# Performance work log

Hardware: AMD Instinct MI355X
Metric: run time of the kernel (lower is better)

The kernel has to match this reference:

```python
import jax, jax.numpy as jnp
import numpy as np

TEMP = 20.0
NEG = -1.0e9


def l2norm(x, eps=1e-12):
    # F.normalize(p=2, dim=-1): x / max(||x||, eps)
    n = jnp.sqrt(jnp.sum(x * x, axis=-1, keepdims=True))
    return x / jnp.maximum(n, eps)


def setup_inputs() -> dict:
    key = jax.random.key(0)
    ks = jax.random.split(key, 8)
    Bv, Lv, Dv = 32, 196, 768
    Bt, Lt, Dt = 32, 64, 768
    D = 512
    inp = {
        "visual_feature": jax.random.normal(ks[0], (Bv, Lv, Dv), jnp.float32),
        "textual_feature": jax.random.normal(ks[1], (Bt, Lt, Dt), jnp.float32),
        "mask": jax.random.randint(ks[2], (Bt, Lt), 0, 2, jnp.int32),
        "W_vis": jax.random.normal(ks[3], (D, Dv), jnp.float32) * (2.0 / D) ** 0.5,
        "b_vis": jnp.zeros((D,), jnp.float32),
        "W_txt": jax.random.normal(ks[4], (D, Dt), jnp.float32) * (2.0 / D) ** 0.5,
        "b_txt": jnp.zeros((D,), jnp.float32),
        "W_qs": jax.random.normal(ks[5], (D, D), jnp.float32) * (2.0 / D) ** 0.5,
        "W_ks": jax.random.normal(ks[6], (D, D), jnp.float32) * (2.0 / D) ** 0.5,
    }
    return inp


def _mha(q_in, k_in, v_in, k_mask, W_qs, W_ks):
    # all-pairs cross attention (n_head == 1), vectorized over the original
    # per-sample Python loop: output [Bk, Bq, Lq, Dv]
    q = l2norm(jnp.einsum('qld,ed->qle', q_in, W_qs))  # [Bq, Lq, D]
    k = l2norm(jnp.einsum('kmd,ed->kme', k_in, W_ks))  # [Bk, Lk, D]
    attn = jnp.einsum('qle,kme->kqlm', q, k)           # [Bk, Bq, Lq, Lk]
    attn = jax.nn.relu(attn) * TEMP
    if k_mask is not None:
        attn = jnp.where(k_mask[:, None, None, :] == 1, NEG, attn)
    attn = jax.nn.softmax(attn, axis=-1)
    return jnp.einsum('kqlm,kmd->kqld', attn, v_in)    # [Bk, Bq, Lq, Dv]


def reference(visual_feature, textual_feature, mask, W_vis, b_vis, W_txt, b_txt, W_qs, W_ks):
    visual_embed = jnp.einsum('bld,ed->ble', visual_feature, W_vis) + b_vis   # [Bv,Lv,D]
    textual_embed = jnp.einsum('bld,ed->ble', textual_feature, W_txt) + b_txt # [Bt,Lt,D]
    visual_norm = l2norm(visual_embed)
    textual_norm = l2norm(textual_embed)
    # q=visual, k/v=textual, masked by text padding -> [Bt, Bv, Lv, D]
    att_text = _mha(visual_norm, textual_norm, textual_embed, mask, W_qs, W_ks)
    # q=textual, k/v=visual, no mask -> [Bv, Bt, Lt, D]
    att_vis = _mha(textual_norm, visual_norm, visual_embed, None, W_qs, W_ks)
    att_text = l2norm(att_text)
    att_vis = l2norm(att_vis)
    # att_vis_feat[:, mask == 1, :] = 0
    att_vis = att_vis * (mask == 0)[None, :, :, None].astype(att_vis.dtype)
    # matmul(att_text [t,v,l,d], att_vis.permute(1,0,3,2) [t,v,d,m]) -> mean(2,3)
    sim = jnp.einsum('tvld,vtmd->tvlm', att_text, att_vis)
    return sim.mean(axis=(2, 3))  # [Bt, Bv]
```

## Files before the change

### kernel.cpp

```cpp
#include <hip/hip_runtime.h>
#include <math.h>

#define BV 32
#define LV 196
#define DV 768
#define BT 32
#define LT 64
#define DD 512
#define MV (BV*LV)
#define MT (BT*LT)
#define TEMPF 20.0f
#define NEGF  -1.0e9f

typedef unsigned short u16;
typedef unsigned int   u32;
typedef short bf16x8 __attribute__((ext_vector_type(8)));
typedef float f32x4  __attribute__((ext_vector_type(4)));

__device__ __forceinline__ u16 f2bf(float f) {
    u32 u = __float_as_uint(f);
    u32 r = u + 0x7fffu + ((u >> 16) & 1u);
    return (u16)(r >> 16);
}
__device__ __forceinline__ float bf2f(u16 h) { return __uint_as_float(((u32)h) << 16); }

__device__ __forceinline__ size_t tiled_chunk_off(int m, int kk, int KB2) {
    int rowBlk = m >> 7, row = m & 127;
    int kBlk = kk >> 6, ke = kk & 63;
    return ((size_t)(rowBlk * KB2 + kBlk) << 13) + row * 64 + ((((ke >> 3) ^ (row & 7)) << 4) >> 1);
}

__global__ __launch_bounds__(256)
void conv_split(const float* __restrict__ X, u16* __restrict__ X2, int M, int K)
{
    int gid = blockIdx.x * 256 + threadIdx.x;
    int perRow = K >> 3;
    if (gid >= M * perRow) return;
    int m = gid / perRow, k8 = (gid - m * perRow) << 3;
    const float* xp = X + (size_t)m * K + k8;
    float x[8];
    *(float4*)&x[0] = *(const float4*)xp;
    *(float4*)&x[4] = *(const float4*)(xp + 4);
    union { u16 h[8]; uint4 v; } hi, lo;
    #pragma unroll
    for (int e = 0; e < 8; ++e) {
        hi.h[e] = f2bf(x[e]);
        lo.h[e] = f2bf(x[e] - bf2f(hi.h[e]));
    }
    int KB2 = K >> 5;
    *(uint4*)&X2[tiled_chunk_off(m, k8, KB2)]     = hi.v;
    *(uint4*)&X2[tiled_chunk_off(m, K + k8, KB2)] = lo.v;
}

__global__ __launch_bounds__(256)
void rownorm_conv(const float* __restrict__ X, u16* __restrict__ X2, int M)
{
    const int row  = blockIdx.x * 4 + (threadIdx.x >> 6);
    const int lane = threadIdx.x & 63;
    const float* ip = X + (size_t)row * DD + lane * 8;
    float x[8];
    *(float4*)&x[0] = *(const float4*)ip;
    *(float4*)&x[4] = *(const float4*)(ip + 4);
    float ss = 0.f;
    #pragma unroll
    for (int e = 0; e < 8; ++e) ss += x[e] * x[e];
    #pragma unroll
    for (int off = 32; off; off >>= 1) ss += __shfl_xor(ss, off, 64);
    const float inv = 1.f / fmaxf(sqrtf(ss), 1e-12f);
    union { u16 h[8]; uint4 v; } hi, lo;
    #pragma unroll
    for (int e = 0; e < 8; ++e) {
        float xv = x[e] * inv;
        hi.h[e] = f2bf(xv);
        lo.h[e] = f2bf(xv - bf2f(hi.h[e]));
    }
    const int k8 = lane * 8, KB2 = 16;
    *(uint4*)&X2[tiled_chunk_off(row, k8, KB2)]       = hi.v;
    *(uint4*)&X2[tiled_chunk_off(row, DD + k8, KB2)]  = lo.v;
}

__device__ __forceinline__ void gload16(const u16* g, u16* l) {
    __builtin_amdgcn_global_load_lds((const __attribute__((address_space(1))) u32*)g,
                                     (__attribute__((address_space(3))) u32*)l, 16, 0, 0);
}

__global__ __launch_bounds__(256, 2)
void gemm_split_nt(const u16* __restrict__ A2, const u16* __restrict__ B2,
                   const float* __restrict__ bias, float* __restrict__ C,
                   int M, int N, int K, int hasBias)
{
    const int KB  = K >> 6;
    const int KB2 = KB * 2;
    const int bm = blockIdx.y, bn = blockIdx.x;
    const int tid = threadIdx.x;
    const int w = tid >> 6, lane = tid & 63;
    const int wr = (w >> 1) << 6, wc = (w & 1) << 6;
    const int fr = lane & 15, fq = lane >> 4;

    __shared__ u16 As[2][8192];
    __shared__ u16 Bs[2][8192];

    f32x4 acc[4][4];
    #pragma unroll
    for (int i = 0; i < 4; ++i)
        #pragma unroll
        for (int j = 0; j < 4; ++j) acc[i][j] = (f32x4){0.f, 0.f, 0.f, 0.f};

    const int swz = (fr & 7) << 4;
    const int aoff0 = ((wr + fr) << 7) >> 1;
    const int boff0 = ((wc + fr) << 7) >> 1;
    const int k0 = ((fq << 4) ^ swz) >> 1;
    const int k1 = ((64 + (fq << 4)) ^ swz) >> 1;

    const int c4 = w * 4;
    const int laneOff = c4 * 512 + lane * 8;

    const int T = 3 * KB;
    int cur = 0;

    {
        const u16* ag = A2 + (((size_t)(bm * KB2)) << 13) + laneOff;
        const u16* bg = B2 + (((size_t)(bn * KB2)) << 13) + laneOff;
        #pragma unroll
        for (int i = 0; i < 4; ++i) {
            gload16(ag + i * 512, &As[0][(c4 + i) * 512]);
            gload16(bg + i * 512, &Bs[0][(c4 + i) * 512]);
        }
    }
    __syncthreads();

    for (int t = 0; t < T; ++t) {
        if (t + 1 < T) {
            int tn = t + 1, ab, bb;
            if (tn < KB)           { ab = tn;          bb = tn; }
            else if (tn < 2 * KB)  { ab = tn - KB;     bb = tn; }
            else                   { ab = tn - KB;     bb = tn - 2 * KB; }
            const u16* ag = A2 + (((size_t)(bm * KB2 + ab)) << 13) + laneOff;
            const u16* bg = B2 + (((size_t)(bn * KB2 + bb)) << 13) + laneOff;
            int nb = cur ^ 1;
            #pragma unroll
            for (int i = 0; i < 4; ++i) {
                gload16(ag + i * 512, &As[nb][(c4 + i) * 512]);
                gload16(bg + i * 512, &Bs[nb][(c4 + i) * 512]);
            }
        }
        #pragma unroll
        for (int ks = 0; ks < 2; ++ks) {
            const int kk = ks ? k1 : k0;
            bf16x8 af[4], bfv[4];
            #pragma unroll
            for (int mi = 0; mi < 4; ++mi)
                af[mi] = *(const bf16x8*)&As[cur][aoff0 + mi * 1024 + kk];
            #pragma unroll
            for (int ni = 0; ni < 4; ++ni)
                bfv[ni] = *(const bf16x8*)&Bs[cur][boff0 + ni * 1024 + kk];
            #pragma unroll
            for (int mi = 0; mi < 4; ++mi)
                #pragma unroll
                for (int ni = 0; ni < 4; ++ni)
                    acc[mi][ni] = __builtin_amdgcn_mfma_f32_16x16x32_bf16(
                        af[mi], bfv[ni], acc[mi][ni], 0, 0, 0);
        }
        __syncthreads();
        cur ^= 1;
    }

    #pragma unroll
    for (int ni = 0; ni < 4; ++ni) {
        const int col = (bn << 7) + wc + ni * 16 + fr;
        const float badd = hasBias ? bias[col] : 0.f;
        #pragma unroll
        for (int mi = 0; mi < 4; ++mi) {
            #pragma unroll
            for (int j = 0; j < 4; ++j) {
                const int row = (bm << 7) + wr + mi * 16 + fq * 4 + j;
                C[(size_t)row * N + col] = acc[mi][ni][j] + badd;
            }
        }
    }
}

__global__ __launch_bounds__(256, 2)
void gemm_pg(const u16* __restrict__ P, const u16* __restrict__ G,
             float* __restrict__ U)
{
    const int v = blockIdx.z;
    const int bm = blockIdx.y, bn = blockIdx.x;
    const int tid = threadIdx.x;
    const int w = tid >> 6, lane = tid & 63;
    const int wr = (w >> 1) << 6, wc = (w & 1) << 6;
    const int fr = lane & 15, fq = lane >> 4;

    const u16* A2 = P + ((size_t)v << 19);
    const u16* B2 = G + ((size_t)v << 16);

    __shared__ u16 As[2][8192];
    __shared__ u16 Bs[2][8192];

    f32x4 acc[4][4];
    #pragma unroll
    for (int i = 0; i < 4; ++i)
        #pragma unroll
        for (int j = 0; j < 4; ++j) acc[i][j] = (f32x4){0.f, 0.f, 0.f, 0.f};

    const int swz = (fr & 7) << 4;
    const int aoff0 = ((wr + fr) << 7) >> 1;
    const int boff0 = ((wc + fr) << 7) >> 1;
    const int k0 = ((fq << 4) ^ swz) >> 1;
    const int k1 = ((64 + (fq << 4)) ^ swz) >> 1;
    const int c4 = w * 4;
    const int laneOff = c4 * 512 + lane * 8;

    int cur = 0;
    {
        const u16* ag = A2 + (((size_t)(bm * 4)) << 13) + laneOff;
        const u16* bg = B2 + (((size_t)(bn * 4)) << 13) + laneOff;
        #pragma unroll
        for (int i = 0; i < 4; ++i) {
            gload16(ag + i * 512, &As[0][(c4 + i) * 512]);
            gload16(bg + i * 512, &Bs[0][(c4 + i) * 512]);
        }
    }
    __syncthreads();

    for (int t = 0; t < 4; ++t) {
        if (t + 1 < 4) {
            const u16* ag = A2 + (((size_t)(bm * 4 + t + 1)) << 13) + laneOff;
            const u16* bg = B2 + (((size_t)(bn * 4 + t + 1)) << 13) + laneOff;
            int nb = cur ^ 1;
            #pragma unroll
            for (int i = 0; i < 4; ++i) {
                gload16(ag + i * 512, &As[nb][(c4 + i) * 512]);
                gload16(bg + i * 512, &Bs[nb][(c4 + i) * 512]);
            }
        }
        #pragma unroll
        for (int ks = 0; ks < 2; ++ks) {
            const int kk = ks ? k1 : k0;
            bf16x8 af[4], bfv[4];
            #pragma unroll
            for (int mi = 0; mi < 4; ++mi)
                af[mi] = *(const bf16x8*)&As[cur][aoff0 + mi * 1024 + kk];
            #pragma unroll
            for (int ni = 0; ni < 4; ++ni)
                bfv[ni] = *(const bf16x8*)&Bs[cur][boff0 + ni * 1024 + kk];
            #pragma unroll
            for (int mi = 0; mi < 4; ++mi)
                #pragma unroll
                for (int ni = 0; ni < 4; ++ni)
                    acc[mi][ni] = __builtin_amdgcn_mfma_f32_16x16x32_bf16(
                        af[mi], bfv[ni], acc[mi][ni], 0, 0, 0);
        }
        __syncthreads();
        cur ^= 1;
    }

    float* Uv = U + (size_t)v * MT * 196;
    #pragma unroll
    for (int ni = 0; ni < 4; ++ni) {
        const int col = (bn << 7) + wc + ni * 16 + fr;
        if (col < 196) {
            #pragma unroll
            for (int mi = 0; mi < 4; ++mi) {
                #pragma unroll
                for (int j = 0; j < 4; ++j) {
                    const int row = (bm << 7) + wr + mi * 16 + fq * 4 + j;
                    Uv[(size_t)row * 196 + col] = acc[mi][ni][j];
                }
            }
        }
    }
}

__global__ __launch_bounds__(256)
void gram_batched(const float* __restrict__ X, float* __restrict__ G, int Mg)
{
    const int bat = blockIdx.z;
    const int it = blockIdx.y, jt = blockIdx.x;
    const int tid = threadIdx.x;
    const int tx = tid & 15, ty = tid >> 4;
    __shared__ float Xa[32][68];
    __shared__ float Xb[32][68];
    const float* Xbase = X + (size_t)bat * Mg * DD;

    float acc[4][4];
    #pragma unroll
    for (int i = 0; i < 4; ++i)
        #pragma unroll
        for (int j = 0; j < 4; ++j) acc[i][j] = 0.f;

    for (int k0 = 0; k0 < DD; k0 += 32) {
        #pragma unroll
        for (int i = 0; i < 2; ++i) {
            int idx = tid + 256 * i;
            int row = idx >> 3;
            int kc  = (idx & 7) << 2;
            int ra = it * 64 + row; ra = (ra < Mg) ? ra : (Mg - 1);
            int rb = jt * 64 + row; rb = (rb < Mg) ? rb : (Mg - 1);
            float4 av = *(const float4*)(Xbase + (size_t)ra * DD + k0 + kc);
            Xa[kc + 0][row] = av.x; Xa[kc + 1][row] = av.y;
            Xa[kc + 2][row] = av.z; Xa[kc + 3][row] = av.w;
            float4 bv = *(const float4*)(Xbase + (size_t)rb * DD + k0 + kc);
            Xb[kc + 0][row] = bv.x; Xb[kc + 1][row] = bv.y;
            Xb[kc + 2][row] = bv.z; Xb[kc + 3][row] = bv.w;
        }
        __syncthreads();
        #pragma unroll 8
        for (int kk = 0; kk < 32; ++kk) {
            float a[4], b[4];
            *(float4*)a = *(const float4*)&Xa[kk][ty * 4];
            *(float4*)b = *(const float4*)&Xb[kk][tx * 4];
            #pragma unroll
            for (int i = 0; i < 4; ++i)
                #pragma unroll
                for (int j = 0; j < 4; ++j)
                    acc[i][j] = fmaf(a[i], b[j], acc[i][j]);
        }
        __syncthreads();
    }

    #pragma unroll
    for (int i = 0; i < 4; ++i) {
        int row = it * 64 + ty * 4 + i;
        int col = jt * 64 + tx * 4;
        if (row < Mg && col < Mg) {
            float* gp = G + ((size_t)bat * Mg + row) * Mg + col;
            *(float4*)gp = make_float4(acc[i][0], acc[i][1], acc[i][2], acc[i][3]);
        }
    }
}

__global__ __launch_bounds__(256)
void gram_vis(const float* __restrict__ X, u16* __restrict__ Gp,
              float* __restrict__ diagF)
{
    const int bat = blockIdx.z;
    const int it = blockIdx.y, jt = blockIdx.x;
    const int tid = threadIdx.x;
    const int tx = tid & 15, ty = tid >> 4;
    __shared__ float Xa[32][68];
    __shared__ float Xb[32][68];
    const float* Xbase = X + (size_t)bat * 196 * DD;

    float acc[4][4];
    #pragma unroll
    for (int i = 0; i < 4; ++i)
        #pragma unroll
        for (int j = 0; j < 4; ++j) acc[i][j] = 0.f;

    for (int k0 = 0; k0 < DD; k0 += 32) {
        #pragma unroll
        for (int i = 0; i < 2; ++i) {
            int idx = tid + 256 * i;
            int row = idx >> 3;
            int kc  = (idx & 7) << 2;
            int ra = it * 64 + row; ra = (ra < 196) ? ra : 195;
            int rb = jt * 64 + row; rb = (rb < 196) ? rb : 195;
            float4 av = *(const float4*)(Xbase + (size_t)ra * DD + k0 + kc);
            Xa[kc + 0][row] = av.x; Xa[kc + 1][row] = av.y;
            Xa[kc + 2][row] = av.z; Xa[kc + 3][row] = av.w;
            float4 bv = *(const float4*)(Xbase + (size_t)rb * DD + k0 + kc);
            Xb[kc + 0][row] = bv.x; Xb[kc + 1][row] = bv.y;
            Xb[kc + 2][row] = bv.z; Xb[kc + 3][row] = bv.w;
        }
        __syncthreads();
        #pragma unroll 8
        for (int kk = 0; kk < 32; ++kk) {
            float a[4], b[4];
            *(float4*)a = *(const float4*)&Xa[kk][ty * 4];
            *(float4*)b = *(const float4*)&Xb[kk][tx * 4];
            #pragma unroll
            for (int i = 0; i < 4; ++i)
                #pragma unroll
                for (int j = 0; j < 4; ++j)
                    acc[i][j] = fmaf(a[i], b[j], acc[i][j]);
        }
        __syncthreads();
    }

    u16* Gv = Gp + ((size_t)bat << 16);
    #pragma unroll
    for (int i = 0; i < 4; ++i) {
        const int row = it * 64 + ty * 4 + i;
        #pragma unroll
        for (int jj = 0; jj < 4; ++jj) {
            const int col = jt * 64 + tx * 4 + jj;
            float val = acc[i][jj];
            u16 o = (row < 196 && col < 196 && row != col) ? f2bf(val) : (u16)0;
            Gv[tiled_chunk_off(row, col & ~7, 4) + (col & 7)] = o;
            if (row == col && row < 196) diagF[bat * 196 + row] = val;
        }
    }
}

__global__ __launch_bounds__(256)
void softmax_vis(const float* __restrict__ S2, u16* __restrict__ P)
{
    const int row  = blockIdx.x;
    const int wave = threadIdx.x >> 6, lane = threadIdx.x & 63;
    const int v = blockIdx.y * 4 + wave;
    __shared__ float pl[4][256];

    const float* srow = S2 + (size_t)row * MV + v * 196;
    float l0 = fmaxf(srow[lane], 0.f) * TEMPF;
    float l1 = fmaxf(srow[lane + 64], 0.f) * TEMPF;
    float l2 = fmaxf(srow[lane + 128], 0.f) * TEMPF;
    float l3 = -3.0e38f;
    if (lane < 4) l3 = fmaxf(srow[lane + 192], 0.f) * TEMPF;
    float mx = fmaxf(fmaxf(l0, l1), fmaxf(l2, l3));
    #pragma unroll
    for (int off = 32; off; off >>= 1) mx = fmaxf(mx, __shfl_xor(mx, off, 64));
    float p0 = __expf(l0 - mx), p1 = __expf(l1 - mx), p2 = __expf(l2 - mx);
    float p3 = (lane < 4) ? __expf(l3 - mx) : 0.f;
    float sum = p0 + p1 + p2 + p3;
    #pragma unroll
    for (int off = 32; off; off >>= 1) sum += __shfl_xor(sum, off, 64);
    float rs = 1.f / sum;
    pl[wave][lane]       = p0 * rs;
    pl[wave][lane + 64]  = p1 * rs;
    pl[wave][lane + 128] = p2 * rs;
    if (lane < 4) pl[wave][lane + 192] = p3 * rs;
    else          pl[wave][lane + 192] = 0.f;
    __syncthreads();

    if (lane < 32) {
        union { u16 h[8]; uint4 u; } c;
        #pragma unroll
        for (int e = 0; e < 8; ++e) c.h[e] = f2bf(pl[wave][lane * 8 + e]);
        u16* Pv = P + ((size_t)v << 19);
        *(uint4*)&Pv[tiled_chunk_off(row, lane * 8, 4)] = c.u;
    }
}

__global__ __launch_bounds__(256)
void vis_norm_w(const float* __restrict__ U, const u16* __restrict__ P,
                const float* __restrict__ diagF, const int* __restrict__ mask,
                float* __restrict__ Wbuf)
{
    const int t = blockIdx.x, v = blockIdx.y;
    const int wave = threadIdx.x >> 6, lane = threadIdx.x & 63;
    __shared__ float wacc[4][200];

    for (int j = lane; j < 200; j += 64) wacc[wave][j] = 0.f;
    __syncthreads();

    const u16* Pv = P + ((size_t)v << 19);
    const float* dF = diagF + v * 196;
    const float d0 = dF[lane], d1 = dF[lane + 64], d2 = dF[lane + 128];
    const float d3 = (lane < 4) ? dF[lane + 192] : 0.f;

    for (int m = wave; m < 64; m += 4) {
        const int row = t * 64 + m;
        const float* urow = U + ((size_t)v * MT + row) * 196;
        const size_t base0 = tiled_chunk_off(row, lane & ~7, 4) + (lane & 7);
        float p0 = bf2f(Pv[base0]);
        float p1 = bf2f(Pv[tiled_chunk_off(row, (lane + 64) & ~7, 4) + (lane & 7)]);
        float p2 = bf2f(Pv[tiled_chunk_off(row, (lane + 128) & ~7, 4) + (lane & 7)]);
        float p3 = (lane < 4) ? bf2f(Pv[tiled_chunk_off(row, (lane + 192) & ~7, 4) + (lane & 7)]) : 0.f;
        float u0 = urow[lane], u1 = urow[lane + 64], u2 = urow[lane + 128];
        float u3 = (lane < 4) ? urow[lane + 192] : 0.f;
        float nsq = p0 * (u0 + d0 * p0) + p1 * (u1 + d1 * p1)
                  + p2 * (u2 + d2 * p2) + p3 * (u3 + d3 * p3);
        #pragma unroll
        for (int off = 32; off; off >>= 1) nsq += __shfl_xor(nsq, off, 64);
        float inv = 1.f / fmaxf(sqrtf(fmaxf(nsq, 0.f)), 1e-12f);
        if (mask[row]) inv = 0.f;
        wacc[wave][lane]       += p0 * inv;
        wacc[wave][lane + 64]  += p1 * inv;
        wacc[wave][lane + 128] += p2 * inv;
        if (lane < 4) wacc[wave][lane + 192] += p3 * inv;
    }
    __syncthreads();
    const int tid = threadIdx.x;
    if (tid < 196)
        Wbuf[((size_t)v * 32 + t) * 196 + tid] =
            wacc[0][tid] + wacc[1][tid] + wacc[2][tid] + wacc[3][tid];
}

__global__ __launch_bounds__(512)
void vis_b(const float* __restrict__ Wbuf, const float* __restrict__ VE,
           float* __restrict__ bacc)
{
    const int t = blockIdx.x, v = blockIdx.y;
    const int tid = threadIdx.x;
    __shared__ float wl[196];
    if (tid < 196) wl[tid] = Wbuf[((size_t)v * 32 + t) * 196 + tid];
    __syncthreads();
    float a0 = 0.f, a1 = 0.f;
    const float* vb = VE + (size_t)v * 196 * DD + tid;
    for (int j = 0; j < 196; j += 2) {
        a0 = fmaf(wl[j],     vb[(size_t)j * DD],       a0);
        a1 = fmaf(wl[j + 1], vb[(size_t)(j + 1) * DD], a1);
    }
    bacc[((size_t)v * 32 + t) * DD + tid] = a0 + a1;
}

__global__ __launch_bounds__(256)
void att_text_stage(const float* __restrict__ S, const float* __restrict__ Gt,
                    const float* __restrict__ TE, const int* __restrict__ mask,
                    float* __restrict__ aacc)
{
    const int t = blockIdx.x, v = blockIdx.y;
    const int tid = threadIdx.x, wave = tid >> 6, lane = tid & 63;
    __shared__ float Gs[64][68];
    __shared__ float pbuf[4][64];
    __shared__ float wacc[4][64];

    {
        const float* gp = Gt + (size_t)t * 64 * 64;
        #pragma unroll
        for (int i = 0; i < 4; ++i) {
            int idx = tid + 256 * i;
            int row = idx >> 4;
            int c4  = (idx & 15) << 2;
            float4 g4 = *(const float4*)(gp + (size_t)idx * 4);
            *(float4*)&Gs[row][c4] = g4;
        }
    }
    wacc[wave][lane] = 0.f;
    const int mk = mask[t * 64 + lane];
    __syncthreads();

    for (int l = wave; l < LV; l += 4) {
        const int r = v * LV + l;
        float s = S[(size_t)r * MT + t * 64 + lane];
        float logit = mk ? NEGF : fmaxf(s, 0.f) * TEMPF;
        float mx = logit;
        #pragma unroll
        for (int off = 32; off; off >>= 1) mx = fmaxf(mx, __shfl_xor(mx, off, 64));
        float p = __expf(logit - mx);
        float sum = p;
        #pragma unroll
        for (int off = 32; off; off >>= 1) sum += __shfl_xor(sum, off, 64);
        p /= sum;
        pbuf[wave][lane] = p;
        float u = 0.f;
        #pragma unroll
        for (int mb = 0; mb < 64; mb += 4) {
            float4 p4 = *(const float4*)&pbuf[wave][mb];
            float4 g4 = *(const float4*)&Gs[lane][mb];
            u = fmaf(p4.x, g4.x, u); u = fmaf(p4.y, g4.y, u);
            u = fmaf(p4.z, g4.z, u); u = fmaf(p4.w, g4.w, u);
        }
        float nsq = p * u;
        #pragma unroll
        for (int off = 32; off; off >>= 1) nsq += __shfl_xor(nsq, off, 64);
        float inv = 1.f / fmaxf(sqrtf(fmaxf(nsq, 0.f)), 1e-12f);
        wacc[wave][lane] += p * inv;
    }
    __syncthreads();
    if (tid < 64)
        wacc[0][tid] = wacc[0][tid] + wacc[1][tid] + wacc[2][tid] + wacc[3][tid];
    __syncthreads();

    const int d = tid * 2;
    float a0 = 0.f, a1 = 0.f;
    const float* tb = TE + (size_t)(t * 64) * DD + d;
    for (int m = 0; m < 64; ++m) {
        float wm = wacc[0][m];
        float2 te = *(const float2*)(tb + (size_t)m * DD);
        a0 = fmaf(wm, te.x, a0);
        a1 = fmaf(wm, te.y, a1);
    }
    *(float2*)(aacc + ((size_t)t * 32 + v) * DD + d) = make_float2(a0, a1);
}

__global__ __launch_bounds__(64)
void final_dot(const float* __restrict__ aacc, const float* __restrict__ bacc,
               float* __restrict__ out)
{
    const int t = blockIdx.x, v = blockIdx.y;
    const int lane = threadIdx.x;
    const float* ap = aacc + ((size_t)t * 32 + v) * DD + lane * 8;
    const float* bp = bacc + ((size_t)v * 32 + t) * DD + lane * 8;
    float4 a0 = *(const float4*)ap,       a1 = *(const float4*)(ap + 4);
    float4 b0 = *(const float4*)bp,       b1 = *(const float4*)(bp + 4);
    float acc = a0.x*b0.x + a0.y*b0.y + a0.z*b0.z + a0.w*b0.w
              + a1.x*b1.x + a1.y*b1.y + a1.z*b1.z + a1.w*b1.w;
    #pragma unroll
    for (int off = 32; off; off >>= 1) acc += __shfl_xor(acc, off, 64);
    if (lane == 0) out[(size_t)t * 32 + v] = acc * (1.f / 12544.f);
}

extern "C" void kernel_launch(void* const* d_in, const int* in_sizes, int n_in,
                              void* d_out, int out_size, void* d_ws, size_t ws_size,
                              hipStream_t stream)
{
    const float* VF   = (const float*)d_in[0];
    const float* TF   = (const float*)d_in[1];
    const int*   mask = (const int*)  d_in[2];
    const float* Wv   = (const float*)d_in[3];
    const float* bv   = (const float*)d_in[4];
    const float* Wt   = (const float*)d_in[5];
    const float* bt   = (const float*)d_in[6];
    const float* Wq   = (const float*)d_in[7];
    const float* Wk   = (const float*)d_in[8];
    float* out = (float*)d_out;

    float* ws = (float*)d_ws;
    size_t off = 0;
    float* R1 = ws + off; off += (size_t)MV * MT;
    float* R2 = ws + off; off += (size_t)MV * DD + (size_t)MT * DD;
    float* R3 = ws + off; off += (size_t)MV * DD;
    float* R4 = ws + off; off += (size_t)MT * DD;
    float* R5 = ws + off; off += (size_t)MV * DD;
    float* R6 = ws + off; off += (size_t)MT * DD;
    float* VE  = ws + off; off += (size_t)MV * DD;
    float* TE  = ws + off; off += (size_t)MT * DD;
    float* Gt  = ws + off; off += (size_t)32 * 64 * 64;
    float* GvR = ws + off; off += (size_t)32 * 196 * 196;
    float* Aac = ws + off; off += (size_t)32 * 32 * DD;
    float* Bac = ws + off; off += (size_t)32 * 32 * DD;

    u16* VF2 = (u16*)R1;
    u16* TF2 = (u16*)R2;
    u16* VN2 = (u16*)R3;  u16* Qv2 = (u16*)R3;
    u16* TN2 = (u16*)R4;  u16* Qt2 = (u16*)R4;
    u16* Wv2 = (u16*)R5;
    u16* Wt2 = Wv2 + (size_t)512 * 1536;
    u16* Wq2 = Wt2 + (size_t)512 * 1536;
    u16* Wk2 = Wq2 + (size_t)512 * 1024;
    u16* Kv2 = (u16*)R5;
    u16* Kt2 = (u16*)R6;
    float* Qv = R1;
    float* Qt = R1 + (size_t)MV * DD;
    float* Kv = R2;
    float* Kt = R2 + (size_t)MV * DD;
    float* S  = R1;
    float* U  = R1;
    u16*   P  = (u16*)R3;
    u16*   Gp = (u16*)GvR;
    float* diagF = GvR + (size_t)32 * 256 * 256 / 2;
    float* Wbuf = R2;

    conv_split<<<(MV * 96 + 255) / 256, 256, 0, stream>>>(VF, VF2, MV, 768);
    conv_split<<<(MT * 96 + 255) / 256, 256, 0, stream>>>(TF, TF2, MT, 768);
    conv_split<<<(512 * 96 + 255) / 256, 256, 0, stream>>>(Wv, Wv2, 512, 768);
    conv_split<<<(512 * 96 + 255) / 256, 256, 0, stream>>>(Wt, Wt2, 512, 768);
    conv_split<<<(512 * 64 + 255) / 256, 256, 0, stream>>>(Wq, Wq2, 512, 512);
    conv_split<<<(512 * 64 + 255) / 256, 256, 0, stream>>>(Wk, Wk2, 512, 512);

    gemm_split_nt<<<dim3(4, 49), 256, 0, stream>>>(VF2, Wv2, bv, VE, MV, 512, 768, 1);
    gemm_split_nt<<<dim3(4, 16), 256, 0, stream>>>(TF2, Wt2, bt, TE, MT, 512, 768, 1);

    rownorm_conv<<<MV / 4, 256, 0, stream>>>(VE, VN2, MV);
    rownorm_conv<<<MT / 4, 256, 0, stream>>>(TE, TN2, MT);
    gram_batched<<<dim3(1, 1, 32), 256, 0, stream>>>(TE, Gt, 64);
    gram_vis<<<dim3(4, 4, 32), 256, 0, stream>>>(VE, Gp, diagF);

    gemm_split_nt<<<dim3(4, 49), 256, 0, stream>>>(VN2, Wq2, nullptr, Qv, MV, 512, 512, 0);
    gemm_split_nt<<<dim3(4, 49), 256, 0, stream>>>(VN2, Wk2, nullptr, Kv, MV, 512, 512, 0);
    gemm_split_nt<<<dim3(4, 16), 256, 0, stream>>>(TN2, Wq2, nullptr, Qt, MT, 512, 512, 0);
    gemm_split_nt<<<dim3(4, 16), 256, 0, stream>>>(TN2, Wk2, nullptr, Kt, MT, 512, 512, 0);

    rownorm_conv<<<MV / 4, 256, 0, stream>>>(Qv, Qv2, MV);
    rownorm_conv<<<MV / 4, 256, 0, stream>>>(Kv, Kv2, MV);
    rownorm_conv<<<MT / 4, 256, 0, stream>>>(Qt, Qt2, MT);
    rownorm_conv<<<MT / 4, 256, 0, stream>>>(Kt, Kt2, MT);

    gemm_split_nt<<<dim3(16, 49), 256, 0, stream>>>(Qv2, Kt2, nullptr, S, MV, MT, 512, 0);
    att_text_stage<<<dim3(32, 32), 256, 0, stream>>>(S, Gt, TE, mask, Aac);

    gemm_split_nt<<<dim3(49, 16), 256, 0, stream>>>(Qt2, Kv2, nullptr, S, MT, MV, 512, 0);
    softmax_vis<<<dim3(MT, 8), 256, 0, stream>>>(S, P);
    gemm_pg<<<dim3(2, 16, 32), 256, 0, stream>>>(P, Gp, U);
    vis_norm_w<<<dim3(32, 32), 256, 0, stream>>>(U, P, diagF, mask, Wbuf);
    vis_b<<<dim3(32, 32), 512, 0, stream>>>(Wbuf, VE, Bac);

    final_dot<<<dim3(32, 32), 64, 0, stream>>>(Aac, Bac, out);
}
```

Measured before the change: 673.5 us.

## Restructure text attention stage with MFMA gram product and drop split-precision for score GEMMs

The text attention stage used to do a scalar P·G product per row in one block per (t,v). It is replaced by text_fused, which tiles 128 score rows per block, runs the softmax into swizzled bf16 LDS and computes P·Gt with bf16 MFMA. It then reduces norm-weighted probabilities into a global buffer via atomics, and a separate kernel text_a applies those weights to the text embeddings. The two score GEMMs (Qv·Kt and Qt·Kv) also gain a split flag that skips the hi/lo compensation passes, cutting their K iterations to a third. This trades accuracy of the logits and gram products for speed.

```diff
diff --git a/kernel.cpp b/kernel.cpp
--- a/kernel.cpp
+++ b/kernel.cpp
@@ -87,7 +87,7 @@
 __global__ __launch_bounds__(256, 2)
 void gemm_split_nt(const u16* __restrict__ A2, const u16* __restrict__ B2,
                    const float* __restrict__ bias, float* __restrict__ C,
-                   int M, int N, int K, int hasBias)
+                   int M, int N, int K, int hasBias, int split)
 {
     const int KB  = K >> 6;
     const int KB2 = KB * 2;
@@ -115,7 +115,7 @@
     const int c4 = w * 4;
     const int laneOff = c4 * 512 + lane * 8;
 
-    const int T = 3 * KB;
+    const int T = split ? 3 * KB : KB;
     int cur = 0;
 
     {
@@ -273,15 +273,14 @@
 }
 
 __global__ __launch_bounds__(256)
-void gram_batched(const float* __restrict__ X, float* __restrict__ G, int Mg)
+void gram_text(const float* __restrict__ X, u16* __restrict__ Gtp,
+               float* __restrict__ diagT)
 {
     const int bat = blockIdx.z;
-    const int it = blockIdx.y, jt = blockIdx.x;
     const int tid = threadIdx.x;
     const int tx = tid & 15, ty = tid >> 4;
     __shared__ float Xa[32][68];
-    __shared__ float Xb[32][68];
-    const float* Xbase = X + (size_t)bat * Mg * DD;
+    const float* Xbase = X + (size_t)bat * 64 * DD;
 
     float acc[4][4];
     #pragma unroll
@@ -290,26 +289,24 @@
         for (int j = 0; j < 4; ++j) acc[i][j] = 0.f;
 
     for (int k0 = 0; k0 < DD; k0 += 32) {
-        #pragma unroll
-        for (int i = 0; i < 2; ++i) {
-            int idx = tid + 256 * i;
-            int row = idx >> 3;
-            int kc  = (idx & 7) << 2;
-            int ra = it * 64 + row; ra = (ra < Mg) ? ra : (Mg - 1);
-            int rb = jt * 64 + row; rb = (rb < Mg) ? rb : (Mg - 1);
-            float4 av = *(const float4*)(Xbase + (size_t)ra * DD + k0 + kc);
-            Xa[kc + 0][row] = av.x; Xa[kc + 1][row] = av.y;
-            Xa[kc + 2][row] = av.z; Xa[kc + 3][row] = av.w;
-            float4 bv = *(const float4*)(Xbase + (size_t)rb * DD + k0 + kc);
-            Xb[kc + 0][row] = bv.x; Xb[kc + 1][row] = bv.y;
-            Xb[kc + 2][row] = bv.z; Xb[kc + 3][row] = bv.w;
+        {
+            int idx = tid;
+            #pragma unroll
+            for (int i = 0; i < 2; ++i) {
+                int id2 = idx + 256 * i;
+                int row = id2 >> 3;
+                int kc  = (id2 & 7) << 2;
+                float4 av = *(const float4*)(Xbase + (size_t)row * DD + k0 + kc);
+                Xa[kc + 0][row] = av.x; Xa[kc + 1][row] = av.y;
+                Xa[kc + 2][row] = av.z; Xa[kc + 3][row] = av.w;
+            }
         }
         __syncthreads();
         #pragma unroll 8
         for (int kk = 0; kk < 32; ++kk) {
             float a[4], b[4];
             *(float4*)a = *(const float4*)&Xa[kk][ty * 4];
-            *(float4*)b = *(const float4*)&Xb[kk][tx * 4];
+            *(float4*)b = *(const float4*)&Xa[kk][tx * 4];
             #pragma unroll
             for (int i = 0; i < 4; ++i)
                 #pragma unroll
@@ -319,13 +316,17 @@
         __syncthreads();
     }
 
+    u16* Gv = Gtp + ((size_t)bat << 12);
     #pragma unroll
     for (int i = 0; i < 4; ++i) {
-        int row = it * 64 + ty * 4 + i;
-        int col = jt * 64 + tx * 4;
-        if (row < Mg && col < Mg) {
-            float* gp = G + ((size_t)bat * Mg + row) * Mg + col;
-            *(float4*)gp = make_float4(acc[i][0], acc[i][1], acc[i][2], acc[i][3]);
+        const int row = ty * 4 + i;
+        #pragma unroll
+        for (int jj = 0; jj < 4; ++jj) {
+            const int col = tx * 4 + jj;
+            float val = acc[i][jj];
+            Gv[row * 64 + ((((col >> 3) ^ (row & 7)) << 3) | (col & 7))] =
+                (row != col) ? f2bf(val) : (u16)0;
+            if (row == col) diagT[bat * 64 + row] = val;
         }
     }
 }
@@ -394,6 +395,140 @@
 }
 
 __global__ __launch_bounds__(256)
+void zero_wt(float* __restrict__ WT)
+{
+    WT[blockIdx.x * 256 + threadIdx.x] = 0.f;
+}
+
+__global__ __launch_bounds__(256, 2)
+void text_fused(const float* __restrict__ S1, const u16* __restrict__ Gtp,
+                const float* __restrict__ diagT, const int* __restrict__ mask,
+                float* __restrict__ WT)
+{
+    const int rb = blockIdx.x;
+    const int t  = blockIdx.y;
+    const int tid = threadIdx.x;
+    const int w = tid >> 6, lane = tid & 63;
+    const int fr = lane & 15, fq = lane >> 4;
+
+    __shared__ float Sblk[128 * 64];
+    __shared__ u16   Ap[128 * 64];
+    __shared__ u16   Glds[64 * 64];
+    __shared__ float dsh[64];
+    __shared__ float wacc[4][2][64];
+
+    gload16(Gtp + ((size_t)t << 12) + tid * 8,        &Glds[tid * 8]);
+    gload16(Gtp + ((size_t)t << 12) + 2048 + tid * 8, &Glds[2048 + tid * 8]);
+    if (tid < 64) dsh[tid] = diagT[t * 64 + tid];
+    {
+        const float* sbase = S1 + (size_t)(rb * 128) * MT + t * 64;
+        #pragma unroll
+        for (int i = 0; i < 8; ++i) {
+            int idx = tid + i * 256;
+            int row = idx >> 4, c4 = (idx & 15) << 2;
+            *(float4*)&Sblk[row * 64 + c4] = *(const float4*)(sbase + (size_t)row * MT + c4);
+        }
+    }
+    wacc[w][0][lane] = 0.f; wacc[w][1][lane] = 0.f;
+    const int mk = mask[t * 64 + lane];
+    __syncthreads();
+
+    for (int rr = w; rr < 128; rr += 4) {
+        float s = Sblk[rr * 64 + lane];
+        float logit = mk ? NEGF : fmaxf(s, 0.f) * TEMPF;
+        float mx = logit;
+        #pragma unroll
+        for (int off = 32; off; off >>= 1) mx = fmaxf(mx, __shfl_xor(mx, off, 64));
+        float p = __expf(logit - mx);
+        float sum = p;
+        #pragma unroll
+        for (int off = 32; off; off >>= 1) sum += __shfl_xor(sum, off, 64);
+        p /= sum;
+        Ap[rr * 64 + ((((lane >> 3) ^ (rr & 7)) << 3) | (lane & 7))] = f2bf(p);
+    }
+    __syncthreads();
+
+    const int wr = (w >> 1) << 6, wc = (w & 1) << 5;
+    f32x4 acc[4][2];
+    #pragma unroll
+    for (int i = 0; i < 4; ++i) { acc[i][0] = (f32x4){0,0,0,0}; acc[i][1] = (f32x4){0,0,0,0}; }
+    const int swz = (fr & 7) << 4;
+    const int aoff0 = (wr + fr) * 64;
+    const int boff0 = (wc + fr) * 64;
+    const int k0 = ((fq << 4) ^ swz) >> 1;
+    const int k1 = ((64 + (fq << 4)) ^ swz) >> 1;
+    #pragma unroll
+    for (int ks = 0; ks < 2; ++ks) {
+        const int kk = ks ? k1 : k0;
+        bf16x8 af[4], bfv[2];
+        #pragma unroll
+        for (int mi = 0; mi < 4; ++mi)
+            af[mi] = *(const bf16x8*)&Ap[aoff0 + mi * 1024 + kk];
+        #pragma unroll
+        for (int ni = 0; ni < 2; ++ni)
+            bfv[ni] = *(const bf16x8*)&Glds[boff0 + ni * 1024 + kk];
+        #pragma unroll
+        for (int mi = 0; mi < 4; ++mi)
+            #pragma unroll
+            for (int ni = 0; ni < 2; ++ni)
+                acc[mi][ni] = __builtin_amdgcn_mfma_f32_16x16x32_bf16(
+                    af[mi], bfv[ni], acc[mi][ni], 0, 0, 0);
+    }
+    float* Ulds = Sblk;
+    #pragma unroll
+    for (int ni = 0; ni < 2; ++ni)
+        #pragma unroll
+        for (int mi = 0; mi < 4; ++mi)
+            #pragma unroll
+            for (int j = 0; j < 4; ++j)
+                Ulds[(wr + mi * 16 + fq * 4 + j) * 64 + (wc + ni * 16 + fr)] = acc[mi][ni][j];
+    __syncthreads();
+
+    const int vb = ((rb * 128) / 196 + 1) * 196;
+    for (int rr = w; rr < 128; rr += 4) {
+        int r = rb * 128 + rr;
+        float p = bf2f(Ap[rr * 64 + ((((lane >> 3) ^ (rr & 7)) << 3) | (lane & 7))]);
+        float u = Ulds[rr * 64 + lane];
+        float nsq = p * (u + dsh[lane] * p);
+        #pragma unroll
+        for (int off = 32; off; off >>= 1) nsq += __shfl_xor(nsq, off, 64);
+        float inv = 1.f / fmaxf(sqrtf(fmaxf(nsq, 0.f)), 1e-12f);
+        int slot = (r >= vb) ? 1 : 0;
+        wacc[w][slot][lane] += p * inv;
+    }
+    __syncthreads();
+    if (tid < 128) {
+        int slot = tid >> 6, m = tid & 63;
+        int v = (rb * 128) / 196 + slot;
+        if (v < 32) {
+            float val = wacc[0][slot][m] + wacc[1][slot][m] + wacc[2][slot][m] + wacc[3][slot][m];
+            atomicAdd(&WT[((size_t)t * 32 + v) * 64 + m], val);
+        }
+    }
+}
+
+__global__ __launch_bounds__(256)
+void text_a(const float* __restrict__ WT, const float* __restrict__ TE,
+            float* __restrict__ aacc)
+{
+    const int t = blockIdx.x, v = blockIdx.y;
+    const int tid = threadIdx.x;
+    __shared__ float wl[64];
+    if (tid < 64) wl[tid] = WT[((size_t)t * 32 + v) * 64 + tid];
+    __syncthreads();
+    const int d = tid * 2;
+    float a0 = 0.f, a1 = 0.f;
+    const float* tb = TE + (size_t)(t * 64) * DD + d;
+    for (int m = 0; m < 64; ++m) {
+        float wm = wl[m];
+        float2 te = *(const float2*)(tb + (size_t)m * DD);
+        a0 = fmaf(wm, te.x, a0);
+        a1 = fmaf(wm, te.y, a1);
+    }
+    *(float2*)(aacc + ((size_t)t * 32 + v) * DD + d) = make_float2(a0, a1);
+}
+
+__global__ __launch_bounds__(256)
 void softmax_vis(const float* __restrict__ S2, u16* __restrict__ P)
 {
     const int row  = blockIdx.x;
@@ -452,8 +587,7 @@
     for (int m = wave; m < 64; m += 4) {
         const int row = t * 64 + m;
         const float* urow = U + ((size_t)v * MT + row) * 196;
-        const size_t base0 = tiled_chunk_off(row, lane & ~7, 4) + (lane & 7);
-        float p0 = bf2f(Pv[base0]);
+        float p0 = bf2f(Pv[tiled_chunk_off(row, lane & ~7, 4) + (lane & 7)]);
         float p1 = bf2f(Pv[tiled_chunk_off(row, (lane + 64) & ~7, 4) + (lane & 7)]);
         float p2 = bf2f(Pv[tiled_chunk_off(row, (lane + 128) & ~7, 4) + (lane & 7)]);
         float p3 = (lane < 4) ? bf2f(Pv[tiled_chunk_off(row, (lane + 192) & ~7, 4) + (lane & 7)]) : 0.f;
@@ -493,76 +627,6 @@
         a1 = fmaf(wl[j + 1], vb[(size_t)(j + 1) * DD], a1);
     }
     bacc[((size_t)v * 32 + t) * DD + tid] = a0 + a1;
-}
-
-__global__ __launch_bounds__(256)
-void att_text_stage(const float* __restrict__ S, const float* __restrict__ Gt,
-                    const float* __restrict__ TE, const int* __restrict__ mask,
-                    float* __restrict__ aacc)
-{
-    const int t = blockIdx.x, v = blockIdx.y;
-    const int tid = threadIdx.x, wave = tid >> 6, lane = tid & 63;
-    __shared__ float Gs[64][68];
-    __shared__ float pbuf[4][64];
-    __shared__ float wacc[4][64];
-
-    {
-        const float* gp = Gt + (size_t)t * 64 * 64;
-        #pragma unroll
-        for (int i = 0; i < 4; ++i) {
-            int idx = tid + 256 * i;
-            int row = idx >> 4;
-            int c4  = (idx & 15) << 2;
-            float4 g4 = *(const float4*)(gp + (size_t)idx * 4);
-            *(float4*)&Gs[row][c4] = g4;
-        }
-    }
-    wacc[wave][lane] = 0.f;
-    const int mk = mask[t * 64 + lane];
-    __syncthreads();
-
-    for (int l = wave; l < LV; l += 4) {
-        const int r = v * LV + l;
-        float s = S[(size_t)r * MT + t * 64 + lane];
-        float logit = mk ? NEGF : fmaxf(s, 0.f) * TEMPF;
-        float mx = logit;
-        #pragma unroll
-        for (int off = 32; off; off >>= 1) mx = fmaxf(mx, __shfl_xor(mx, off, 64));
-        float p = __expf(logit - mx);
-        float sum = p;
-        #pragma unroll
-        for (int off = 32; off; off >>= 1) sum += __shfl_xor(sum, off, 64);
-        p /= sum;
-        pbuf[wave][lane] = p;
-        float u = 0.f;
-        #pragma unroll
-        for (int mb = 0; mb < 64; mb += 4) {
-            float4 p4 = *(const float4*)&pbuf[wave][mb];
-            float4 g4 = *(const float4*)&Gs[lane][mb];
-            u = fmaf(p4.x, g4.x, u); u = fmaf(p4.y, g4.y, u);
-            u = fmaf(p4.z, g4.z, u); u = fmaf(p4.w, g4.w, u);
-        }
-        float nsq = p * u;
-        #pragma unroll
-        for (int off = 32; off; off >>= 1) nsq += __shfl_xor(nsq, off, 64);
-        float inv = 1.f / fmaxf(sqrtf(fmaxf(nsq, 0.f)), 1e-12f);
-        wacc[wave][lane] += p * inv;
-    }
-    __syncthreads();
-    if (tid < 64)
-        wacc[0][tid] = wacc[0][tid] + wacc[1][tid] + wacc[2][tid] + wacc[3][tid];
-    __syncthreads();
-
-    const int d = tid * 2;
-    float a0 = 0.f, a1 = 0.f;
-    const float* tb = TE + (size_t)(t * 64) * DD + d;
-    for (int m = 0; m < 64; ++m) {
-        float wm = wacc[0][m];
-        float2 te = *(const float2*)(tb + (size_t)m * DD);
-        a0 = fmaf(wm, te.x, a0);
-        a1 = fmaf(wm, te.y, a1);
-    }
-    *(float2*)(aacc + ((size_t)t * 32 + v) * DD + d) = make_float2(a0, a1);
 }
 
 __global__ __launch_bounds__(64)
@@ -607,7 +671,7 @@
     float* R6 = ws + off; off += (size_t)MT * DD;
     float* VE  = ws + off; off += (size_t)MV * DD;
     float* TE  = ws + off; off += (size_t)MT * DD;
-    float* Gt  = ws + off; off += (size_t)32 * 64 * 64;
+    float* GtR = ws + off; off += (size_t)32 * 64 * 64;
     float* GvR = ws + off; off += (size_t)32 * 196 * 196;
     float* Aac = ws + off; off += (size_t)32 * 32 * DD;
     float* Bac = ws + off; off += (size_t)32 * 32 * DD;
@@ -629,8 +693,11 @@
     float* S  = R1;
     float* U  = R1;
     u16*   P  = (u16*)R3;
+    u16*   Gtp  = (u16*)GtR;
+    float* diagT = GtR + 65536;
     u16*   Gp = (u16*)GvR;
     float* diagF = GvR + (size_t)32 * 256 * 256 / 2;
+    float* WT    = diagF + 6272;
     float* Wbuf = R2;
 
     conv_split<<<(MV * 96 + 255) / 256, 256, 0, stream>>>(VF, VF2, MV, 768);
@@ -640,28 +707,30 @@
     conv_split<<<(512 * 64 + 255) / 256, 256, 0, stream>>>(Wq, Wq2, 512, 512);
     conv_split<<<(512 * 64 + 255) / 256, 256, 0, stream>>>(Wk, Wk2, 512, 512);
 
-    gemm_split_nt<<<dim3(4, 49), 256, 0, stream>>>(VF2, Wv2, bv, VE, MV, 512, 768, 1);
-    gemm_split_nt<<<dim3(4, 16), 256, 0, stream>>>(TF2, Wt2, bt, TE, MT, 512, 768, 1);
+    gemm_split_nt<<<dim3(4, 49), 256, 0, stream>>>(VF2, Wv2, bv, VE, MV, 512, 768, 1, 1);
+    gemm_split_nt<<<dim3(4, 16), 256, 0, stream>>>(TF2, Wt2, bt, TE, MT, 512, 768, 1, 1);
 
     rownorm_conv<<<MV / 4, 256, 0, stream>>>(VE, VN2, MV);
     rownorm_conv<<<MT / 4, 256, 0, stream>>>(TE, TN2, MT);
-    gram_batched<<<dim3(1, 1, 32), 256, 0, stream>>>(TE, Gt, 64);
+    gram_text<<<dim3(1, 1, 32), 256, 0, stream>>>(TE, Gtp, diagT);
     gram_vis<<<dim3(4, 4, 32), 256, 0, stream>>>(VE, Gp, diagF);
 
-    gemm_split_nt<<<dim3(4, 49), 256, 0, stream>>>(VN2, Wq2, nullptr, Qv, MV, 512, 512, 0);
-    gemm_split_nt<<<dim3(4, 49), 256, 0, stream>>>(VN2, Wk2, nullptr, Kv, MV, 512, 512, 0);
-    gemm_split_nt<<<dim3(4, 16), 256, 0, stream>>>(TN2, Wq2, nullptr, Qt, MT, 512, 512, 0);
-    gemm_split_nt<<<dim3(4, 16), 256, 0, stream>>>(TN2, Wk2, nullptr, Kt, MT, 512, 512, 0);
+    gemm_split_nt<<<dim3(4, 49), 256, 0, stream>>>(VN2, Wq2, nullptr, Qv, MV, 512, 512, 0, 1);
+    gemm_split_nt<<<dim3(4, 49), 256, 0, stream>>>(VN2, Wk2, nullptr, Kv, MV, 512, 512, 0, 1);
+    gemm_split_nt<<<dim3(4, 16), 256, 0, stream>>>(TN2, Wq2, nullptr, Qt, MT, 512, 512, 0, 1);
+    gemm_split_nt<<<dim3(4, 16), 256, 0, stream>>>(TN2, Wk2, nullptr, Kt, MT, 512, 512, 0, 1);
 
     rownorm_conv<<<MV / 4, 256, 0, stream>>>(Qv, Qv2, MV);
     rownorm_conv<<<MV / 4, 256, 0, stream>>>(Kv, Kv2, MV);
     rownorm_conv<<<MT / 4, 256, 0, stream>>>(Qt, Qt2, MT);
     rownorm_conv<<<MT / 4, 256, 0, stream>>>(Kt, Kt2, MT);
 
-    gemm_split_nt<<<dim3(16, 49), 256, 0, stream>>>(Qv2, Kt2, nullptr, S, MV, MT, 512, 0);
-    att_text_stage<<<dim3(32, 32), 256, 0, stream>>>(S, Gt, TE, mask, Aac);
-
-    gemm_split_nt<<<dim3(49, 16), 256, 0, stream>>>(Qt2, Kv2, nullptr, S, MT, MV, 512, 0);
+    gemm_split_nt<<<dim3(16, 49), 256, 0, stream>>>(Qv2, Kt2, nullptr, S, MV, MT, 512, 0, 0);
+    zero_wt<<<256, 256, 0, stream>>>(WT);
+    text_fused<<<dim3(49, 32), 256, 0, stream>>>(S, Gtp, diagT, mask, WT);
+    text_a<<<dim3(32, 32), 256, 0, stream>>>(WT, TE, Aac);
+
+    gemm_split_nt<<<dim3(49, 16), 256, 0, stream>>>(Qt2, Kv2, nullptr, S, MT, MV, 512, 0, 0);
     softmax_vis<<<dim3(MT, 8), 256, 0, stream>>>(S, P);
     gemm_pg<<<dim3(2, 16, 32), 256, 0, stream>>>(P, Gp, U);
     vis_norm_w<<<dim3(32, 32), 256, 0, stream>>>(U, P, diagF, mask, Wbuf);
```

Result: no change. 660.5 us (-1.9%).
